# Performance work log

Hardware: AMD Instinct MI355X
Metric: run time of the kernel (lower is better)

Reference implementation:

```python
import jax, jax.numpy as jnp
import numpy as np

DEPTH = 4  # 2**DEPTH - 1 = 15 decision nodes, 2**DEPTH = 16 leaves


def setup_inputs() -> dict:
    key = jax.random.key(0)
    k1, k2, k3, k4, k5 = jax.random.split(key, 5)
    B, S, H = 2, 2048, 1024
    n_dec, n_leaf = 2 ** DEPTH - 1, 2 ** DEPTH
    s = 1.0 / np.sqrt(H)
    return {
        "x": jax.random.normal(k1, (B, S, H), dtype=jnp.float32),
        "Wd": jax.random.normal(k2, (n_dec, H, 2), dtype=jnp.float32) * s,
        "bd": jax.random.normal(k3, (n_dec, 2), dtype=jnp.float32) * s,
        "Wl": jax.random.normal(k4, (n_leaf, H, H), dtype=jnp.float32) * s,
        "bl": jax.random.normal(k5, (n_leaf, H), dtype=jnp.float32) * s,
    }


def reference(x, Wd, bd, Wl, bl):
    B, S, H = x.shape
    # All decision nodes in one grouped GEMM: [B,S,n_dec,2], independent sigmoids
    decisions = jax.nn.sigmoid(jnp.einsum('bsh,nhk->bsnk', x, Wd) + bd)
    # Cumulative path probabilities with torch-faithful cat([p*left, p*right]) ordering
    path = jnp.ones((B, S, 1), dtype=x.dtype)
    for level in range(DEPTH):
        start = 2 ** level - 1
        lv = decisions[:, :, start:start + 2 ** level, :]  # [B,S,2^level,2]
        path = jnp.concatenate([path * lv[..., 0], path * lv[..., 1]], axis=-1)
    # Weighted leaf-output sum without materializing [B,S,n_leaf,H]
    out = jnp.einsum('bsh,lhd,bsl->bsd', x, Wl, path, optimize=True)
    out = out + jnp.einsum('bsl,ld->bsd', path, bl)
    return out
```

## Files before the change

### kernel.cpp

```cpp
#include <hip/hip_runtime.h>
#include <hip/hip_bf16.h>

typedef unsigned short u16;
typedef unsigned int u32;
typedef short bf16x8 __attribute__((ext_vector_type(8)));
typedef _Float16 f16x8 __attribute__((ext_vector_type(8)));
typedef float f32x4 __attribute__((ext_vector_type(4)));

__device__ __forceinline__ u16 f2bf(float f) {
    u32 u = __builtin_bit_cast(u32, f);
    u32 r = (u + 0x7FFFu + ((u >> 16) & 1u)) >> 16;
    return (u16)r;
}
__device__ __forceinline__ u16 f2h(float f) {
    _Float16 h = (_Float16)f;
    return __builtin_bit_cast(u16, h);
}

__device__ __forceinline__ void lds16(const void* g, void* s) {
    __builtin_amdgcn_global_load_lds(
        (const __attribute__((address_space(1))) u32*)g,
        (__attribute__((address_space(3))) u32*)s, 16, 0, 0);
}

__global__ __launch_bounds__(256) void path_kernel(
    const float* __restrict__ x, const float* __restrict__ Wd,
    const float* __restrict__ bd, float* __restrict__ path,
    u16* __restrict__ xb, int as_f16, int M) {
    int lane = threadIdx.x & 63;
    int wid = threadIdx.x >> 6;
    int m = blockIdx.x * 4 + wid;
    if (m >= M) return;

    const float* xr = x + (size_t)m * 1024;
    float v[16];
#pragma unroll
    for (int i = 0; i < 16; ++i) v[i] = xr[lane + 64 * i];
#pragma unroll
    for (int i = 0; i < 16; ++i)
        xb[(size_t)m * 1024 + lane + 64 * i] = as_f16 ? f2h(v[i]) : f2bf(v[i]);

    int leaf = lane & 15;
    int nd[4], bit[4];
#pragma unroll
    for (int k = 0; k < 4; ++k) {
        nd[k] = (1 << k) - 1 + (leaf & ((1 << k) - 1));
        bit[k] = (leaf >> k) & 1;
    }
    float z[4] = {0.f, 0.f, 0.f, 0.f};

    const float2* Wd2 = (const float2*)Wd;
    for (int n = 0; n < 15; ++n) {
        float s0 = 0.f, s1 = 0.f;
#pragma unroll
        for (int i = 0; i < 16; ++i) {
            float2 w = Wd2[n * 1024 + lane + 64 * i];
            s0 += v[i] * w.x;
            s1 += v[i] * w.y;
        }
#pragma unroll
        for (int off = 32; off; off >>= 1) {
            s0 += __shfl_xor(s0, off, 64);
            s1 += __shfl_xor(s1, off, 64);
        }
#pragma unroll
        for (int k = 0; k < 4; ++k)
            if (nd[k] == n) z[k] = bit[k] ? s1 : s0;
    }
    float p = 1.f;
#pragma unroll
    for (int k = 0; k < 4; ++k) {
        float zz = z[k] + bd[nd[k] * 2 + bit[k]];
        p *= 1.f / (1.f + expf(-zz));
    }
    if (lane < 16) path[(size_t)m * 16 + leaf] = p;
}

__global__ __launch_bounds__(256) void wlt_kernel(
    const float* __restrict__ Wl, u16* __restrict__ wlt, int as_f16) {
    __shared__ float tile[64][65];
    int l = blockIdx.z, hb = blockIdx.y, nb = blockIdx.x;
    int t = threadIdx.x;
    int r = t >> 2, cq = (t & 3) << 4;

    const float* src = Wl + ((size_t)(l * 1024 + hb * 64 + r)) * 1024 + nb * 64 + cq;
#pragma unroll
    for (int j = 0; j < 4; ++j) {
        float4 w = ((const float4*)src)[j];
        tile[r][cq + 4 * j + 0] = w.x;
        tile[r][cq + 4 * j + 1] = w.y;
        tile[r][cq + 4 * j + 2] = w.z;
        tile[r][cq + 4 * j + 3] = w.w;
    }
    __syncthreads();
    union { u16 u[16]; uint4 q[2]; } pk;
#pragma unroll
    for (int j = 0; j < 16; ++j)
        pk.u[j] = as_f16 ? f2h(tile[cq + j][r]) : f2bf(tile[cq + j][r]);
    u16* dst = wlt + ((size_t)(l * 1024 + nb * 64 + r)) * 1024 + hb * 64 + cq;
    ((uint4*)dst)[0] = pk.q[0];
    ((uint4*)dst)[1] = pk.q[1];
}

__global__ __launch_bounds__(512, 2) void tree_gemm8(
    const u16* __restrict__ xh, const u16* __restrict__ wlt,
    const float* __restrict__ path, float* __restrict__ out,
    float* __restrict__ part, int M) {
    __shared__ __align__(16) u16 Asm[2][2][128 * 64];
    __shared__ __align__(16) u16 Bsm[2][2][128 * 64];
    __shared__ u16 psm_h[4][256];

    const int tid = threadIdx.x, lane = tid & 63, w = tid >> 6;
    const int wm = w >> 2, wn = w & 3;
    const int nbm = M >> 8;
    int xb_, yb_, zb_;
    {
        int bid = blockIdx.x;
        if ((nbm << 4) == 256) {
            int k = bid & 7, s = bid >> 3;
            zb_ = k >> 1; yb_ = (k & 1) * 8 + (s >> 2); xb_ = s & 3;
        } else {
            xb_ = bid & 3; int t2 = bid >> 2; yb_ = t2 % nbm; zb_ = t2 / nbm;
        }
    }
    const int n0 = xb_ * 256, m0 = yb_ * 256, z = zb_;
    const int z4 = z * 4;
    const int rl = lane >> 3;
    const int srcswz = ((lane & 7) ^ rl) << 4;
    const int arow = (lane & 15) * 128;
    const int coff0 = ((lane >> 4) << 4) ^ ((lane & 7) << 4);

    for (int i = tid; i < 1024; i += 512) {
        int r = i >> 2, lz = i & 3;
        psm_h[lz][r] = f2h(path[(size_t)(m0 + r) * 16 + z4 + lz]);
    }

#define ISSUE_A(dst_, ks_)                                                          \
    {                                                                               \
        _Pragma("unroll") for (int h_ = 0; h_ < 2; ++h_)                            \
        _Pragma("unroll") for (int j_ = 0; j_ < 2; ++j_)                            \
            lds16((const char*)xh +                                                 \
                      (size_t)(m0 + h_ * 128 + w * 16 + j_ * 8 + rl) * 2048 +       \
                      ((ks_) << 7) + srcswz,                                        \
                  (dst_) + h_ * 16384 + w * 2048 + j_ * 1024);                      \
    }
#define ISSUE_B(dst_, t_)                                                           \
    if ((t_) < 64) {                                                                \
        size_t lb_ = (size_t)(z4 + ((t_) & 3)) * 2097152 +                          \
                     ((size_t)((t_) >> 2) << 7);                                    \
        _Pragma("unroll") for (int h_ = 0; h_ < 2; ++h_)                            \
        _Pragma("unroll") for (int j_ = 0; j_ < 2; ++j_)                            \
            lds16((const char*)wlt + lb_ +                                          \
                      (size_t)(n0 + h_ * 128 + w * 16 + j_ * 8 + rl) * 2048 +       \
                      srcswz,                                                       \
                  (dst_) + h_ * 16384 + w * 2048 + j_ * 1024);                      \
    }
#define LDA4(aB_, mfb)                                                              \
    _Pragma("unroll") for (int q_ = 0; q_ < 4; ++q_) {                              \
        aR[q_][0] = *(const f16x8*)((aB_) + ((mfb) + q_) * 2048 + coff0);           \
        aR[q_][1] = *(const f16x8*)((aB_) + ((mfb) + q_) * 2048 + (coff0 ^ 64));    \
    }
#define LDB2(bB_, nfb, d0)                                                          \
    _Pragma("unroll") for (int q_ = 0; q_ < 2; ++q_) {                              \
        bR[(d0) + q_][0] = *(const f16x8*)((bB_) + ((nfb) + q_) * 2048 + coff0);    \
        bR[(d0) + q_][1] =                                                          \
            *(const f16x8*)((bB_) + ((nfb) + q_) * 2048 + (coff0 ^ 64));            \
    }
#define LDP(ll, mfb)                                                                \
    _Pragma("unroll") for (int q_ = 0; q_ < 4; ++q_)                                \
        p2[q_] = __builtin_bit_cast(                                                \
            _Float16, psm_h[ll][wm * 128 + ((mfb) + q_) * 16 + (lane & 15)]);
#define SCALE                                                                       \
    _Pragma("unroll") for (int q_ = 0; q_ < 4; ++q_) {                              \
        aR[q_][0] *= p2[q_];                                                        \
        aR[q_][1] *= p2[q_];                                                        \
    }
#define MM(a0, b0)                                                                  \
    _Pragma("unroll") for (int mq_ = 0; mq_ < 4; ++mq_)                             \
    _Pragma("unroll") for (int nq_ = 0; nq_ < 2; ++nq_) {                           \
        acc[(a0) + mq_][(b0) + nq_] = __builtin_amdgcn_mfma_f32_16x16x32_f16(       \
            aR[mq_][0], bR[(b0) + nq_][0], acc[(a0) + mq_][(b0) + nq_], 0, 0, 0);   \
        acc[(a0) + mq_][(b0) + nq_] = __builtin_amdgcn_mfma_f32_16x16x32_f16(       \
            aR[mq_][1], bR[(b0) + nq_][1], acc[(a0) + mq_][(b0) + nq_], 0, 0, 0);   \
    }
#define BAR __builtin_amdgcn_s_barrier()
#define LG0 asm volatile("s_waitcnt lgkmcnt(0)" ::: "memory")
#define PRIO1 __builtin_amdgcn_s_setprio(1)
#define PRIO0 __builtin_amdgcn_s_setprio(0)
#define VM4 asm volatile("s_waitcnt vmcnt(4)" ::: "memory")
#define VM8 asm volatile("s_waitcnt vmcnt(8)" ::: "memory")
#define VM0 asm volatile("s_waitcnt vmcnt(0)" ::: "memory")
#define NOPX ((void)0)

#define TILE(aB_, bB_, ll, EB2, EA, WT)                                             \
    {                                                                               \
        f16x8 aR[4][2], bR[4][2];                                                   \
        _Float16 p2[4];                                                             \
                                                                      \
        LDA4(aB_, 0); LDB2(bB_, 0, 0); LDP(ll, 0);                                  \
        BAR; LG0; SCALE; PRIO1; MM(0, 0); PRIO0; BAR;                               \
                                                                      \
        LDB2(bB_, 2, 2);                                                            \
        BAR; LG0; PRIO1; MM(0, 2); PRIO0; BAR;                                      \
                         \
        LDA4(aB_, 4); LDP(ll, 4); EB2; EA;                                          \
        BAR; LG0; SCALE; PRIO1; MM(4, 0); PRIO0; BAR;                               \
                                                          \
        PRIO1; MM(4, 2); PRIO0; WT; BAR;                                            \
    }

    f32x4 acc[8][4];
#pragma unroll
    for (int a = 0; a < 8; ++a)
#pragma unroll
        for (int b = 0; b < 4; ++b) acc[a][b] = (f32x4){0.f, 0.f, 0.f, 0.f};

    const char* aBase0 = (const char*)Asm[0][wm] + arow;
    const char* aBase1 = (const char*)Asm[1][wm] + arow;
    const char* bBase0 = (const char*)Bsm[0][wn >> 1] + (wn & 1) * 8192 + arow;
    const char* bBase1 = (const char*)Bsm[1][wn >> 1] + (wn & 1) * 8192 + arow;
    char* aSlot0 = (char*)Asm[0][0];
    char* aSlot1 = (char*)Asm[1][0];
    char* bSlot0 = (char*)Bsm[0][0];
    char* bSlot1 = (char*)Bsm[1][0];

    ISSUE_A(aSlot0, 0);
    ISSUE_B(bSlot0, 0);
    ISSUE_B(bSlot1, 1);
    asm volatile("s_waitcnt vmcnt(4) lgkmcnt(0)" ::: "memory");
    BAR;
    __builtin_amdgcn_sched_barrier(0);

#pragma unroll 1
    for (int ks = 0; ks < 15; ++ks) {
        const int t4 = ks << 2;
        const char* aB = (ks & 1) ? aBase1 : aBase0;
        char* aD = (ks & 1) ? aSlot0 : aSlot1;
        TILE(aB, bBase0, 0, ISSUE_B(bSlot0, t4 + 2), NOPX, VM4);
        TILE(aB, bBase1, 1, ISSUE_B(bSlot1, t4 + 3), ISSUE_A(aD, ks + 1), VM8);
        TILE(aB, bBase0, 2, ISSUE_B(bSlot0, t4 + 4), NOPX, VM8);
        TILE(aB, bBase1, 3, ISSUE_B(bSlot1, t4 + 5), NOPX, VM4);
    }
    {
        const char* aB = aBase1;
        TILE(aB, bBase0, 0, ISSUE_B(bSlot0, 62), NOPX, VM4);
        TILE(aB, bBase1, 1, ISSUE_B(bSlot1, 63), NOPX, VM4);
        TILE(aB, bBase0, 2, NOPX, NOPX, VM0);
        TILE(aB, bBase1, 3, NOPX, NOPX, NOPX);
    }

    float* po = (z == 0) ? out : part + (size_t)(z - 1) * M * 1024;
    const int r0 = m0 + wm * 128 + ((lane >> 4) << 2);
    const int c0 = n0 + wn * 64 + (lane & 15);
#pragma unroll
    for (int mf = 0; mf < 8; ++mf)
#pragma unroll
        for (int jj = 0; jj < 4; ++jj)
#pragma unroll
            for (int nf = 0; nf < 4; ++nf)
                po[(size_t)(r0 + mf * 16 + jj) * 1024 + c0 + nf * 16] = acc[mf][nf][jj];
#undef ISSUE_A
#undef ISSUE_B
#undef LDA4
#undef LDB2
#undef LDP
#undef SCALE
#undef MM
#undef BAR
#undef LG0
#undef PRIO1
#undef PRIO0
#undef VM4
#undef VM8
#undef VM0
#undef NOPX
#undef TILE
}

__global__ __launch_bounds__(256) void tree_gemm_fb(
    const u16* __restrict__ xb, const u16* __restrict__ wlt,
    const float* __restrict__ path, float* __restrict__ pout,
    int M, int LPB, int lgLPB) {
    __shared__ __align__(16) u16 Asm[128 * 64];
    __shared__ __align__(16) u16 Bsm[128 * 64];
    __shared__ float psm[128][16];

    const int tid = threadIdx.x, lane = tid & 63, wid = tid >> 6;
    const int wm = wid >> 1, wn = wid & 1;
    const int m0 = blockIdx.y * 128, n0 = blockIdx.x * 128;
    const int lbase = blockIdx.z * LPB;

    for (int i = tid; i < (128 << lgLPB); i += 256) {
        int r = i >> lgLPB, c = i & (LPB - 1);
        psm[r][c] = path[(size_t)(m0 + r) * 16 + lbase + c];
    }

    const int colb = (((lane & 7) ^ (lane >> 3)) << 4);
    const int rl = lane >> 3;

    f32x4 accF[4][4], accL[4][4];
#pragma unroll
    for (int a = 0; a < 4; ++a)
#pragma unroll
        for (int b = 0; b < 4; ++b) {
            accF[a][b] = (f32x4){0.f, 0.f, 0.f, 0.f};
            accL[a][b] = (f32x4){0.f, 0.f, 0.f, 0.f};
        }

    const int nsteps = LPB << 4;
    for (int sl = 0; sl < nsteps; ++sl) {
        const int l_ = lbase + (sl >> 4);
        const int h2_ = (sl & 15) << 7;
#pragma unroll
        for (int i_ = 0; i_ < 4; ++i_) {
            int seg_ = wid * 4 + i_;
            int r_ = seg_ * 8 + rl;
            lds16((const char*)xb + (size_t)(m0 + r_) * 2048 + h2_ + colb,
                  (char*)Asm + seg_ * 1024);
            lds16((const char*)wlt + (size_t)(l_ * 1024 + n0 + r_) * 2048 + h2_ + colb,
                  (char*)Bsm + seg_ * 1024);
        }
        __syncthreads();

#pragma unroll
        for (int kf = 0; kf < 2; ++kf) {
            int c2 = kf * 64 + ((lane >> 4) << 4);
            bf16x8 af[4], bfr[4];
#pragma unroll
            for (int mf = 0; mf < 4; ++mf) {
                int rr = wm * 64 + mf * 16 + (lane & 15);
                af[mf] = *(const bf16x8*)((const char*)Asm + rr * 128 + (c2 ^ ((lane & 7) << 4)));
            }
#pragma unroll
            for (int nf = 0; nf < 4; ++nf) {
                int rr = wn * 64 + nf * 16 + (lane & 15);
                bfr[nf] = *(const bf16x8*)((const char*)Bsm + rr * 128 + (c2 ^ ((lane & 7) << 4)));
            }
#pragma unroll
            for (int mf = 0; mf < 4; ++mf)
#pragma unroll
                for (int nf = 0; nf < 4; ++nf)
                    accL[mf][nf] = __builtin_amdgcn_mfma_f32_16x16x32_bf16(
                        af[mf], bfr[nf], accL[mf][nf], 0, 0, 0);
        }
        __syncthreads();

        if ((sl & 15) == 15) {
            int ll = sl >> 4;
#pragma unroll
            for (int mf = 0; mf < 4; ++mf)
#pragma unroll
                for (int jj = 0; jj < 4; ++jj) {
                    float p = psm[wm * 64 + mf * 16 + ((lane >> 4) << 2) + jj][ll];
#pragma unroll
                    for (int nf = 0; nf < 4; ++nf) {
                        accF[mf][nf][jj] += p * accL[mf][nf][jj];
                        accL[mf][nf][jj] = 0.f;
                    }
                }
        }
    }

    float* po = pout + (size_t)blockIdx.z * M * 1024;
#pragma unroll
    for (int mf = 0; mf < 4; ++mf)
#pragma unroll
        for (int jj = 0; jj < 4; ++jj) {
            int rowl = wm * 64 + mf * 16 + ((lane >> 4) << 2) + jj;
#pragma unroll
            for (int nf = 0; nf < 4; ++nf) {
                int col = n0 + wn * 64 + nf * 16 + (lane & 15);
                po[(size_t)(m0 + rowl) * 1024 + col] = accF[mf][nf][jj];
            }
        }
}

__global__ __launch_bounds__(256) void reduce_kernel(
    const float* __restrict__ extra, const float* __restrict__ path,
    const float* __restrict__ bl, float* __restrict__ out, int M,
    int nExtra, int readOut) {
    int m = blockIdx.x, t = threadIdx.x;
    size_t i4 = (size_t)m * 256 + t;
    f32x4 acc = {0.f, 0.f, 0.f, 0.f};
    if (readOut) acc = ((const f32x4*)out)[i4];
    for (int g = 0; g < nExtra; ++g)
        acc += ((const f32x4*)extra)[(size_t)g * M * 256 + i4];
#pragma unroll
    for (int l = 0; l < 16; ++l) {
        float p = path[(size_t)m * 16 + l];
        f32x4 b = ((const f32x4*)bl)[l * 256 + t];
        acc += p * b;
    }
    ((f32x4*)out)[i4] = acc;
}

extern "C" void kernel_launch(void* const* d_in, const int* in_sizes, int n_in,
                              void* d_out, int out_size, void* d_ws, size_t ws_size,
                              hipStream_t stream) {
    const float* x  = (const float*)d_in[0];
    const float* Wd = (const float*)d_in[1];
    const float* bd = (const float*)d_in[2];
    const float* Wl = (const float*)d_in[3];
    const float* bl = (const float*)d_in[4];
    float* out = (float*)d_out;

    const int H = 1024;
    const int M = in_sizes[0] / H;
    char* ws = (char*)d_ws;

    size_t n_off_xh   = (size_t)M * 16 * 4;
    size_t n_off_wlt  = n_off_xh + (size_t)M * 1024 * 2;
    size_t n_off_part = n_off_wlt + (size_t)16 * 1024 * 1024 * 2;
    size_t n_need     = n_off_part + 3 * (size_t)M * 1024 * 4;

    if (ws_size >= n_need && (M % 256) == 0) {
        float* path = (float*)ws;
        u16* xh  = (u16*)(ws + n_off_xh);
        u16* wlt = (u16*)(ws + n_off_wlt);
        float* part = (float*)(ws + n_off_part);

        path_kernel<<<M / 4, 256, 0, stream>>>(x, Wd, bd, path, xh, 1, M);
        wlt_kernel<<<dim3(16, 16, 16), 256, 0, stream>>>(Wl, wlt, 1);
        tree_gemm8<<<4 * (M / 256) * 4, 512, 0, stream>>>(xh, wlt, path, out, part, M);
        reduce_kernel<<<M, 256, 0, stream>>>(part, path, bl, out, M, 3, 1);
        return;
    }

    size_t off_xb   = (size_t)M * 16 * 4;
    size_t off_wlt  = off_xb + (size_t)M * 1024 * 2;
    size_t off_part = off_wlt + (size_t)16 * 1024 * 1024 * 2;
    size_t per_part = (size_t)M * 1024 * 4;

    int G = 1;
    if (ws_size >= off_part + 4 * per_part) G = 4;
    else if (ws_size >= off_part + 2 * per_part) G = 2;
    const int LPB = 16 / G;
    const int lgLPB = (G == 1) ? 4 : (G == 2) ? 3 : 2;

    float* path = (float*)ws;
    u16* xb  = (u16*)(ws + off_xb);
    u16* wlt = (u16*)(ws + off_wlt);
    float* pout = (G == 1) ? out : (float*)(ws + off_part);

    path_kernel<<<M / 4, 256, 0, stream>>>(x, Wd, bd, path, xb, 0, M);
    wlt_kernel<<<dim3(16, 16, 16), 256, 0, stream>>>(Wl, wlt, 0);
    tree_gemm_fb<<<dim3(8, M / 128, G), 256, 0, stream>>>(xb, wlt, path, pout, M, LPB, lgLPB);
    reduce_kernel<<<M, 256, 0, stream>>>(pout, path, bl, out, M,
                                         (G == 1) ? 0 : G, (G == 1) ? 1 : 0);
}
```

Before: 202.7 us.

## Merge path and weight-transpose kernels; split A prefetch across tile phases

Folds the weight transpose/convert kernel and the path/x-convert kernel into one launch, with block index ranges selecting the role. This removes a launch and lets the two independent preprocessing jobs run concurrently. Inside the main GEMM, the A-tile prefetch is split into two halves issued at different points of the tile body, and the vmcnt waits are loosened to match the deeper count of outstanding loads. The aim is to spread global-to-LDS traffic more evenly against the MFMA work, at the cost of more fragile wait-count bookkeeping.

```diff
diff --git a/kernel.cpp b/kernel.cpp
--- a/kernel.cpp
+++ b/kernel.cpp
@@ -23,13 +23,42 @@
         (__attribute__((address_space(3))) u32*)s, 16, 0, 0);
 }
 
-__global__ __launch_bounds__(256) void path_kernel(
+__global__ __launch_bounds__(256) void pre_kernel(
     const float* __restrict__ x, const float* __restrict__ Wd,
-    const float* __restrict__ bd, float* __restrict__ path,
-    u16* __restrict__ xb, int as_f16, int M) {
+    const float* __restrict__ bd, const float* __restrict__ Wl,
+    float* __restrict__ path, u16* __restrict__ xb, u16* __restrict__ wlt,
+    int as_f16, int M) {
+    __shared__ float tile[64][65];
+    const int bid = blockIdx.x;
+
+    if (bid < 4096) {
+        int nb = bid & 15, hb = (bid >> 4) & 15, l = bid >> 8;
+        int t = threadIdx.x;
+        int r = t >> 2, cq = (t & 3) << 4;
+
+        const float* src = Wl + ((size_t)(l * 1024 + hb * 64 + r)) * 1024 + nb * 64 + cq;
+#pragma unroll
+        for (int j = 0; j < 4; ++j) {
+            float4 w = ((const float4*)src)[j];
+            tile[r][cq + 4 * j + 0] = w.x;
+            tile[r][cq + 4 * j + 1] = w.y;
+            tile[r][cq + 4 * j + 2] = w.z;
+            tile[r][cq + 4 * j + 3] = w.w;
+        }
+        __syncthreads();
+        union { u16 u[16]; uint4 q[2]; } pk;
+#pragma unroll
+        for (int j = 0; j < 16; ++j)
+            pk.u[j] = as_f16 ? f2h(tile[cq + j][r]) : f2bf(tile[cq + j][r]);
+        u16* dst = wlt + ((size_t)(l * 1024 + nb * 64 + r)) * 1024 + hb * 64 + cq;
+        ((uint4*)dst)[0] = pk.q[0];
+        ((uint4*)dst)[1] = pk.q[1];
+        return;
+    }
+
     int lane = threadIdx.x & 63;
     int wid = threadIdx.x >> 6;
-    int m = blockIdx.x * 4 + wid;
+    int m = (bid - 4096) * 4 + wid;
     if (m >= M) return;
 
     const float* xr = x + (size_t)m * 1024;
@@ -74,32 +103,6 @@
         p *= 1.f / (1.f + expf(-zz));
     }
     if (lane < 16) path[(size_t)m * 16 + leaf] = p;
-}
-
-__global__ __launch_bounds__(256) void wlt_kernel(
-    const float* __restrict__ Wl, u16* __restrict__ wlt, int as_f16) {
-    __shared__ float tile[64][65];
-    int l = blockIdx.z, hb = blockIdx.y, nb = blockIdx.x;
-    int t = threadIdx.x;
-    int r = t >> 2, cq = (t & 3) << 4;
-
-    const float* src = Wl + ((size_t)(l * 1024 + hb * 64 + r)) * 1024 + nb * 64 + cq;
-#pragma unroll
-    for (int j = 0; j < 4; ++j) {
-        float4 w = ((const float4*)src)[j];
-        tile[r][cq + 4 * j + 0] = w.x;
-        tile[r][cq + 4 * j + 1] = w.y;
-        tile[r][cq + 4 * j + 2] = w.z;
-        tile[r][cq + 4 * j + 3] = w.w;
-    }
-    __syncthreads();
-    union { u16 u[16]; uint4 q[2]; } pk;
-#pragma unroll
-    for (int j = 0; j < 16; ++j)
-        pk.u[j] = as_f16 ? f2h(tile[cq + j][r]) : f2bf(tile[cq + j][r]);
-    u16* dst = wlt + ((size_t)(l * 1024 + nb * 64 + r)) * 1024 + hb * 64 + cq;
-    ((uint4*)dst)[0] = pk.q[0];
-    ((uint4*)dst)[1] = pk.q[1];
 }
 
 __global__ __launch_bounds__(512, 2) void tree_gemm8(
@@ -135,15 +138,15 @@
         psm_h[lz][r] = f2h(path[(size_t)(m0 + r) * 16 + z4 + lz]);
     }
 
-#define ISSUE_A(dst_, ks_)                                                          \
+#define ISSUE_A_H(dst_, ks_, h_)                                                    \
     {                                                                               \
-        _Pragma("unroll") for (int h_ = 0; h_ < 2; ++h_)                            \
         _Pragma("unroll") for (int j_ = 0; j_ < 2; ++j_)                            \
             lds16((const char*)xh +                                                 \
-                      (size_t)(m0 + h_ * 128 + w * 16 + j_ * 8 + rl) * 2048 +       \
+                      (size_t)(m0 + (h_) * 128 + w * 16 + j_ * 8 + rl) * 2048 +     \
                       ((ks_) << 7) + srcswz,                                        \
-                  (dst_) + h_ * 16384 + w * 2048 + j_ * 1024);                      \
-    }
+                  (dst_) + (h_) * 16384 + w * 2048 + j_ * 1024);                    \
+    }
+#define ISSUE_A(dst_, ks_) { ISSUE_A_H(dst_, ks_, 0); ISSUE_A_H(dst_, ks_, 1); }
 #define ISSUE_B(dst_, t_)                                                           \
     if ((t_) < 64) {                                                                \
         size_t lb_ = (size_t)(z4 + ((t_) & 3)) * 2097152 +                          \
@@ -187,12 +190,12 @@
 #define LG0 asm volatile("s_waitcnt lgkmcnt(0)" ::: "memory")
 #define PRIO1 __builtin_amdgcn_s_setprio(1)
 #define PRIO0 __builtin_amdgcn_s_setprio(0)
-#define VM4 asm volatile("s_waitcnt vmcnt(4)" ::: "memory")
+#define VM0 asm volatile("s_waitcnt vmcnt(0)" ::: "memory")
 #define VM8 asm volatile("s_waitcnt vmcnt(8)" ::: "memory")
-#define VM0 asm volatile("s_waitcnt vmcnt(0)" ::: "memory")
+#define VM16 asm volatile("s_waitcnt vmcnt(16)" ::: "memory")
 #define NOPX ((void)0)
 
-#define TILE(aB_, bB_, ll, EB2, EA, WT)                                             \
+#define TILE(aB_, bB_, ll, EB2, EA0, EA1, WT)                                       \
     {                                                                               \
         f16x8 aR[4][2], bR[4][2];                                                   \
         _Float16 p2[4];                                                             \
@@ -202,10 +205,11 @@
                                                                       \
         LDB2(bB_, 2, 2);                                                            \
         BAR; LG0; PRIO1; MM(0, 2); PRIO0; BAR;                                      \
-                         \
-        LDA4(aB_, 4); LDP(ll, 4); EB2; EA;                                          \
+                  \
+        LDA4(aB_, 4); LDP(ll, 4); EB2; EA0;                                         \
         BAR; LG0; SCALE; PRIO1; MM(4, 0); PRIO0; BAR;                               \
-                                                          \
+                      \
+        EA1;                                                                        \
         PRIO1; MM(4, 2); PRIO0; WT; BAR;                                            \
     }
 
@@ -227,7 +231,7 @@
     ISSUE_A(aSlot0, 0);
     ISSUE_B(bSlot0, 0);
     ISSUE_B(bSlot1, 1);
-    asm volatile("s_waitcnt vmcnt(4) lgkmcnt(0)" ::: "memory");
+    asm volatile("s_waitcnt vmcnt(8) lgkmcnt(0)" ::: "memory");
     BAR;
     __builtin_amdgcn_sched_barrier(0);
 
@@ -236,17 +240,18 @@
         const int t4 = ks << 2;
         const char* aB = (ks & 1) ? aBase1 : aBase0;
         char* aD = (ks & 1) ? aSlot0 : aSlot1;
-        TILE(aB, bBase0, 0, ISSUE_B(bSlot0, t4 + 2), NOPX, VM4);
-        TILE(aB, bBase1, 1, ISSUE_B(bSlot1, t4 + 3), ISSUE_A(aD, ks + 1), VM8);
-        TILE(aB, bBase0, 2, ISSUE_B(bSlot0, t4 + 4), NOPX, VM8);
-        TILE(aB, bBase1, 3, ISSUE_B(bSlot1, t4 + 5), NOPX, VM4);
+        TILE(aB, bBase0, 0, ISSUE_B(bSlot0, t4 + 2), NOPX, NOPX, VM8);
+        TILE(aB, bBase1, 1, ISSUE_B(bSlot1, t4 + 3),
+             ISSUE_A_H(aD, ks + 1, 0), ISSUE_A_H(aD, ks + 1, 1), VM16);
+        TILE(aB, bBase0, 2, ISSUE_B(bSlot0, t4 + 4), NOPX, NOPX, VM16);
+        TILE(aB, bBase1, 3, ISSUE_B(bSlot1, t4 + 5), NOPX, NOPX, VM8);
     }
     {
         const char* aB = aBase1;
-        TILE(aB, bBase0, 0, ISSUE_B(bSlot0, 62), NOPX, VM4);
-        TILE(aB, bBase1, 1, ISSUE_B(bSlot1, 63), NOPX, VM4);
-        TILE(aB, bBase0, 2, NOPX, NOPX, VM0);
-        TILE(aB, bBase1, 3, NOPX, NOPX, NOPX);
+        TILE(aB, bBase0, 0, ISSUE_B(bSlot0, 62), NOPX, NOPX, VM8);
+        TILE(aB, bBase1, 1, ISSUE_B(bSlot1, 63), NOPX, NOPX, VM8);
+        TILE(aB, bBase0, 2, NOPX, NOPX, NOPX, VM0);
+        TILE(aB, bBase1, 3, NOPX, NOPX, NOPX, NOPX);
     }
 
     float* po = (z == 0) ? out : part + (size_t)(z - 1) * M * 1024;
@@ -259,6 +264,7 @@
 #pragma unroll
             for (int nf = 0; nf < 4; ++nf)
                 po[(size_t)(r0 + mf * 16 + jj) * 1024 + c0 + nf * 16] = acc[mf][nf][jj];
+#undef ISSUE_A_H
 #undef ISSUE_A
 #undef ISSUE_B
 #undef LDA4
@@ -270,9 +276,9 @@
 #undef LG0
 #undef PRIO1
 #undef PRIO0
-#undef VM4
+#undef VM0
 #undef VM8
-#undef VM0
+#undef VM16
 #undef NOPX
 #undef TILE
 }
@@ -419,8 +425,7 @@
         u16* wlt = (u16*)(ws + n_off_wlt);
         float* part = (float*)(ws + n_off_part);
 
-        path_kernel<<<M / 4, 256, 0, stream>>>(x, Wd, bd, path, xh, 1, M);
-        wlt_kernel<<<dim3(16, 16, 16), 256, 0, stream>>>(Wl, wlt, 1);
+        pre_kernel<<<4096 + M / 4, 256, 0, stream>>>(x, Wd, bd, Wl, path, xh, wlt, 1, M);
         tree_gemm8<<<4 * (M / 256) * 4, 512, 0, stream>>>(xh, wlt, path, out, part, M);
         reduce_kernel<<<M, 256, 0, stream>>>(part, path, bl, out, M, 3, 1);
         return;
@@ -442,8 +447,7 @@
     u16* wlt = (u16*)(ws + off_wlt);
     float* pout = (G == 1) ? out : (float*)(ws + off_part);
 
-    path_kernel<<<M / 4, 256, 0, stream>>>(x, Wd, bd, path, xb, 0, M);
-    wlt_kernel<<<dim3(16, 16, 16), 256, 0, stream>>>(Wl, wlt, 0);
+    pre_kernel<<<4096 + (M + 3) / 4, 256, 0, stream>>>(x, Wd, bd, Wl, path, xb, wlt, 0, M);
     tree_gemm_fb<<<dim3(8, M / 128, G), 256, 0, stream>>>(xb, wlt, path, pout, M, LPB, lgLPB);
     reduce_kernel<<<M, 256, 0, stream>>>(pout, path, bl, out, M,
                                          (G == 1) ? 0 : G, (G == 1) ? 1 : 0);
```

Measured after the change: 209.1 us. +3.2%, slower.

## Simplify tile pipeline to one barrier per tile with prefetch distance one

Applied to the files above, without the earlier changes.

Restructures the main GEMM tile macro. Each tile now loads all A/B fragments up front and issues the next global-to-LDS prefetch right away. Four barrier pairs per tile are replaced by waitcnt plus sched_barrier, leaving a single barrier at the end. The B-tile prefetch distance drops from two tiles ahead to one, and the vmcnt waits become vmcnt(0) in most places. This cuts barrier and synchronisation overhead, but it reduces how much memory latency can be hidden behind the MFMA work.

```diff
diff --git a/kernel.cpp b/kernel.cpp
--- a/kernel.cpp
+++ b/kernel.cpp
@@ -185,28 +185,27 @@
     }
 #define BAR __builtin_amdgcn_s_barrier()
 #define LG0 asm volatile("s_waitcnt lgkmcnt(0)" ::: "memory")
+#define SCHED0 __builtin_amdgcn_sched_barrier(0)
 #define PRIO1 __builtin_amdgcn_s_setprio(1)
 #define PRIO0 __builtin_amdgcn_s_setprio(0)
+#define VM0 asm volatile("s_waitcnt vmcnt(0)" ::: "memory")
 #define VM4 asm volatile("s_waitcnt vmcnt(4)" ::: "memory")
-#define VM8 asm volatile("s_waitcnt vmcnt(8)" ::: "memory")
-#define VM0 asm volatile("s_waitcnt vmcnt(0)" ::: "memory")
 #define NOPX ((void)0)
 
-#define TILE(aB_, bB_, ll, EB2, EA, WT)                                             \
+#define TILE(aB_, bB_, ll, EB, EA, WT)                                              \
     {                                                                               \
         f16x8 aR[4][2], bR[4][2];                                                   \
         _Float16 p2[4];                                                             \
-                                                                      \
-        LDA4(aB_, 0); LDB2(bB_, 0, 0); LDP(ll, 0);                                  \
-        BAR; LG0; SCALE; PRIO1; MM(0, 0); PRIO0; BAR;                               \
-                                                                      \
-        LDB2(bB_, 2, 2);                                                            \
-        BAR; LG0; PRIO1; MM(0, 2); PRIO0; BAR;                                      \
-                         \
-        LDA4(aB_, 4); LDP(ll, 4); EB2; EA;                                          \
-        BAR; LG0; SCALE; PRIO1; MM(4, 0); PRIO0; BAR;                               \
-                                                          \
-        PRIO1; MM(4, 2); PRIO0; WT; BAR;                                            \
+        LDA4(aB_, 0); LDB2(bB_, 0, 0); LDB2(bB_, 2, 2); LDP(ll, 0);                 \
+        EB; EA;                                                                     \
+        LG0; SCHED0;                                                                \
+        SCALE;                                                                      \
+        PRIO1; MM(0, 0); MM(0, 2); PRIO0;                                           \
+        LDA4(aB_, 4); LDP(ll, 4);                                                   \
+        LG0; SCHED0;                                                                \
+        SCALE;                                                                      \
+        PRIO1; MM(4, 0); MM(4, 2); PRIO0;                                           \
+        WT; BAR;                                                                    \
     }
 
     f32x4 acc[8][4];
@@ -226,26 +225,25 @@
 
     ISSUE_A(aSlot0, 0);
     ISSUE_B(bSlot0, 0);
-    ISSUE_B(bSlot1, 1);
-    asm volatile("s_waitcnt vmcnt(4) lgkmcnt(0)" ::: "memory");
+    asm volatile("s_waitcnt vmcnt(0) lgkmcnt(0)" ::: "memory");
     BAR;
-    __builtin_amdgcn_sched_barrier(0);
+    SCHED0;
 
 #pragma unroll 1
     for (int ks = 0; ks < 15; ++ks) {
         const int t4 = ks << 2;
         const char* aB = (ks & 1) ? aBase1 : aBase0;
         char* aD = (ks & 1) ? aSlot0 : aSlot1;
-        TILE(aB, bBase0, 0, ISSUE_B(bSlot0, t4 + 2), NOPX, VM4);
-        TILE(aB, bBase1, 1, ISSUE_B(bSlot1, t4 + 3), ISSUE_A(aD, ks + 1), VM8);
-        TILE(aB, bBase0, 2, ISSUE_B(bSlot0, t4 + 4), NOPX, VM8);
-        TILE(aB, bBase1, 3, ISSUE_B(bSlot1, t4 + 5), NOPX, VM4);
+        TILE(aB, bBase0, 0, ISSUE_B(bSlot1, t4 + 1), NOPX, VM0);
+        TILE(aB, bBase1, 1, ISSUE_B(bSlot0, t4 + 2), ISSUE_A(aD, ks + 1), VM4);
+        TILE(aB, bBase0, 2, ISSUE_B(bSlot1, t4 + 3), NOPX, VM0);
+        TILE(aB, bBase1, 3, ISSUE_B(bSlot0, t4 + 4), NOPX, VM0);
     }
     {
         const char* aB = aBase1;
-        TILE(aB, bBase0, 0, ISSUE_B(bSlot0, 62), NOPX, VM4);
-        TILE(aB, bBase1, 1, ISSUE_B(bSlot1, 63), NOPX, VM4);
-        TILE(aB, bBase0, 2, NOPX, NOPX, VM0);
+        TILE(aB, bBase0, 0, ISSUE_B(bSlot1, 61), NOPX, VM0);
+        TILE(aB, bBase1, 1, ISSUE_B(bSlot0, 62), NOPX, VM0);
+        TILE(aB, bBase0, 2, ISSUE_B(bSlot1, 63), NOPX, VM0);
         TILE(aB, bBase1, 3, NOPX, NOPX, NOPX);
     }
 
@@ -268,11 +266,11 @@
 #undef MM
 #undef BAR
 #undef LG0
+#undef SCHED0
 #undef PRIO1
 #undef PRIO0
+#undef VM0
 #undef VM4
-#undef VM8
-#undef VM0
 #undef NOPX
 #undef TILE
 }
```

Result: faster. 197.3 us (-2.7%).
